# Kernel tuning notes

Measured on AMD Instinct MI355X. Metric: run time of the kernel, lower is better.

Reference implementation:

```python
import jax, jax.numpy as jnp
import numpy as np

N_Q = 5000
MEM = 50
KDIM = 50
VDIM = 200
FC = 50
B = 2048
S = 200


def setup_inputs() -> dict:
    key = jax.random.key(0)
    ks = jax.random.split(key, 14)
    inp = {}
    inp["q_data"] = jax.random.randint(ks[0], (B, S), 0, N_Q, dtype=jnp.int64)
    inp["qa_data"] = jax.random.randint(ks[1], (B, S), 0, 2 * N_Q, dtype=jnp.int64)
    # learned parameters (kaiming-ish random init)
    inp["q_embed_w"] = jax.random.normal(ks[2], (N_Q + 1, KDIM), jnp.float32) * 0.2
    inp["qa_embed_w"] = jax.random.normal(ks[3], (2 * N_Q + 1, VDIM), jnp.float32) * 0.1
    inp["key_memory"] = jax.random.normal(ks[4], (MEM, KDIM), jnp.float32) * 0.2
    inp["init_value_memory"] = jax.random.normal(ks[5], (MEM, VDIM), jnp.float32) * 0.1
    # DKVMN write gates: erase (sigmoid) and add (tanh) transforms of qa embedding
    inp["erase_w"] = jax.random.normal(ks[6], (VDIM, VDIM), jnp.float32) * 0.1
    inp["erase_b"] = jnp.zeros((VDIM,), jnp.float32)
    inp["add_w"] = jax.random.normal(ks[7], (VDIM, VDIM), jnp.float32) * 0.1
    inp["add_b"] = jnp.zeros((VDIM,), jnp.float32)
    # prediction MLP: Linear(VDIM+KDIM -> FC), Tanh, Linear(FC -> 1)
    inp["pred_w1"] = jax.random.normal(ks[8], (VDIM + KDIM, FC), jnp.float32) * 0.1
    inp["pred_b1"] = jnp.zeros((FC,), jnp.float32)
    inp["pred_w2"] = jax.random.normal(ks[9], (FC, 1), jnp.float32) * 0.2
    inp["pred_b2"] = jnp.zeros((1,), jnp.float32)
    return inp


def _dkvmn_forward(q_data, qa_data, q_embed_w, qa_embed_w, key_memory,
                   init_value_memory, erase_w, erase_b, add_w, add_b,
                   pred_w1, pred_b1, pred_w2, pred_b2):
    q_emb = q_embed_w[q_data]    # [B, S, KDIM]
    qa_emb = qa_embed_w[qa_data]  # [B, S, VDIM]
    batch = q_data.shape[0]
    Mv0 = jnp.broadcast_to(init_value_memory, (batch, MEM, VDIM))

    def step(Mv, xs):
        q_t, qa_t = xs  # [B, KDIM], [B, VDIM]
        # attention over memory slots
        w = jax.nn.softmax(q_t @ key_memory.T, axis=-1)          # [B, MEM]
        read = jnp.einsum('bm,bmv->bv', w, Mv)                    # [B, VDIM]
        h = jnp.tanh(jnp.concatenate([read, q_t], -1) @ pred_w1 + pred_b1)
        p = jax.nn.sigmoid((h @ pred_w2 + pred_b2)[:, 0])         # [B]
        # erase/add write
        e = jax.nn.sigmoid(qa_t @ erase_w + erase_b)              # [B, VDIM]
        a = jnp.tanh(qa_t @ add_w + add_b)                        # [B, VDIM]
        Mv_new = Mv * (1.0 - w[:, :, None] * e[:, None, :]) + w[:, :, None] * a[:, None, :]
        return Mv_new, p

    xs = (jnp.swapaxes(q_emb, 0, 1), jnp.swapaxes(qa_emb, 0, 1))  # time-major
    _, preds = jax.lax.scan(step, Mv0, xs)                        # [S, B]
    return preds.T                                                # [B, S]


def reference(q_data, qa_data, q_embed_w, qa_embed_w, key_memory,
              init_value_memory, erase_w, erase_b, add_w, add_b,
              pred_w1, pred_b1, pred_w2, pred_b2):
    preds = _dkvmn_forward(q_data, qa_data, q_embed_w, qa_embed_w, key_memory,
                           init_value_memory, erase_w, erase_b, add_w, add_b,
                           pred_w1, pred_b1, pred_w2, pred_b2)
    zeros = jnp.zeros_like(preds)
    return (preds, zeros, zeros, zeros)
```

## Files before the change

kernel.cpp:

```cpp
#include <hip/hip_runtime.h>
#include <hip/hip_fp16.h>


#define NQ1   5001
#define NQA   10001
#define MEMN  50
#define KD    50
#define VD    200
#define FC    50
#define BB    2048
#define SS    200
#define EA_R  16
#define WHS   28

#define EA_B   626
#define WQ_B   1251
#define PACK_B 8
#define PREP_G (EA_B + WQ_B + PACK_B)

typedef unsigned int   u32;
typedef unsigned short u16;
typedef short    s8v __attribute__((ext_vector_type(8)));
typedef float    f4v __attribute__((ext_vector_type(4)));
typedef _Float16 h2v __attribute__((ext_vector_type(2)));

__device__ __forceinline__ float fast_sigmoid(float x) { return 1.f / (1.f + __expf(-x)); }
__device__ __forceinline__ float fast_tanh(float x) {
    float e2 = __expf(2.f * x);
    return 1.f - 2.f / (e2 + 1.f);
}
__device__ __forceinline__ float bfu16_to_f(u16 u) {
    union { float f; u32 i; } x; x.i = ((u32)u) << 16; return x.f;
}
__device__ __forceinline__ u16 f_to_bfu16(float f) {
    union { float f; u32 i; } x; x.f = f;
    return (u16)((x.i + 0x7fffu + ((x.i >> 16) & 1u)) >> 16);
}
__device__ __forceinline__ h2v u32_to_h2v(u32 u) {
    union { u32 i; h2v h; } x; x.i = u; return x.h;
}
__device__ __forceinline__ u16 f16bits(float f) {
    union { __half h; u16 u; } x; x.h = __float2half(f); return x.u;
}
__device__ __forceinline__ float h16_to_f(u16 u) {
    union { u16 u; __half h; } x; x.u = u; return __half2float(x.h);
}

__global__ __launch_bounds__(256) void prep(
        const float* __restrict__ qemb, const float* __restrict__ km,
        const float* __restrict__ w1,   const float* __restrict__ b1,
        const float* __restrict__ qaemb,
        const float* __restrict__ ew,   const float* __restrict__ ebias,
        const float* __restrict__ aw,   const float* __restrict__ abias,
        float* __restrict__ Wt, u32* __restrict__ Wh, float* __restrict__ Q1,
        u32* __restrict__ EA, u16* __restrict__ W1s,
        float* __restrict__ out_aux) {
    const int tid = threadIdx.x;
    const int blk = blockIdx.x;

    for (size_t i = (size_t)blk * 256 + tid; i < 3ull * BB * SS;
         i += (size_t)PREP_G * 256)
        out_aux[i] = 0.f;

    __shared__ float smem[VD * EA_R];

    if (blk < EA_B) {
        const int r0 = blk * EA_R;
        if (tid < VD) {
            #pragma unroll
            for (int r = 0; r < EA_R; ++r) {
                int row = r0 + r;
                smem[tid * EA_R + r] = (row < NQA) ? qaemb[(size_t)row * VD + tid] : 0.f;
            }
        }
        __syncthreads();
        if (tid >= VD) return;

        float accE[EA_R], accA[EA_R];
        #pragma unroll
        for (int r = 0; r < EA_R; ++r) { accE[r] = 0.f; accA[r] = 0.f; }
        for (int k = 0; k < VD; ++k) {
            float we = ew[k * VD + tid];
            float wa = aw[k * VD + tid];
            #pragma unroll
            for (int r = 0; r < EA_R; ++r) {
                float qv = smem[k * EA_R + r];
                accE[r] = fmaf(qv, we, accE[r]);
                accA[r] = fmaf(qv, wa, accA[r]);
            }
        }
        float be = ebias[tid], ba = abias[tid];
        #pragma unroll
        for (int r = 0; r < EA_R; ++r) {
            int row = r0 + r;
            if (row < NQA) {
                u16 ne16 = f16bits(-fast_sigmoid(accE[r] + be));
                u16 a16  = f16bits(fast_tanh(accA[r] + ba));
                EA[(size_t)row * VD + tid] = (u32)ne16 | ((u32)a16 << 16);
            }
        }
    } else if (blk < EA_B + WQ_B) {
        const int lane = tid & 63;
        const int wv   = tid >> 6;
        const int q    = (blk - EA_B) * 4 + wv;
        const bool qok = q < NQ1;
        float* qrow = smem + wv * 64;
        if (qok && lane < KD) qrow[lane] = qemb[q * KD + lane];
        __syncthreads();
        if (!qok) return;

        float s = -1e30f;
        if (lane < MEMN) {
            s = 0.f;
            #pragma unroll
            for (int k = 0; k < KD; ++k) s = fmaf(qrow[k], km[lane * KD + k], s);
        }
        float mx = s;
        #pragma unroll
        for (int off = 32; off >= 1; off >>= 1) mx = fmaxf(mx, __shfl_xor(mx, off, 64));
        float e = (lane < MEMN) ? __expf(s - mx) : 0.f;
        float sum = e;
        #pragma unroll
        for (int off = 32; off >= 1; off >>= 1) sum += __shfl_xor(sum, off, 64);
        float wv_ = (lane < MEMN) ? (e / sum) : 0.f;
        if (lane < MEMN) Wt[q * MEMN + lane] = wv_;

        float plo = __shfl(wv_, 2 * (lane & 31), 64);
        float phi = __shfl(wv_, 2 * (lane & 31) + 1, 64);
        if (lane < 25) {
            Wh[q * WHS + lane] = (u32)f16bits(plo) | ((u32)f16bits(phi) << 16);
        } else if (lane < WHS) {
            Wh[q * WHS + lane] = 0;
        }

        if (lane < FC) {
            float h = b1[lane];
            #pragma unroll
            for (int k = 0; k < KD; ++k)
                h = fmaf(qrow[k], w1[(VD + k) * FC + lane], h);
            Q1[q * FC + lane] = h;
        }
    } else {
        for (int idx = (blk - EA_B - WQ_B) * 256 + tid; idx < 4 * 7 * 64 * 8;
             idx += PACK_B * 256) {
            int j    = idx & 7;
            int lane = (idx >> 3) & 63;
            int kt   = (idx >> 9) % 7;
            int nt   = idx / 3584;
            int k = kt * 32 + ((lane >> 4) << 3) + j;
            int n = nt * 16 + (lane & 15);
            float v = (k < VD && n < FC) ? w1[k * FC + n] : 0.f;
            W1s[idx] = f_to_bfu16(v);
        }
    }
}

__global__ __launch_bounds__(256) void dkvmn_state(
        const int* __restrict__ qd, const int* __restrict__ qad,
        const u32* __restrict__ Wh, const u32* __restrict__ EA,
        const float* __restrict__ ivm, u16* __restrict__ READ) {
    const int tid = threadIdx.x;
    const int b   = blockIdx.x;
    const int v   = tid;
    const bool active = v < VD;
    const int vc = active ? v : VD - 1;

    h2v mv[25];
    #pragma unroll
    for (int i = 0; i < 25; ++i) {
        mv[i].x = (_Float16)ivm[(2 * i) * VD + vc];
        mv[i].y = (_Float16)ivm[(2 * i + 1) * VD + vc];
    }

    const int base = b * SS;
    int q_c = __builtin_amdgcn_readfirstlane(qd[base]);
    int q_n = __builtin_amdgcn_readfirstlane(qd[base + 1]);
    int qa0 = __builtin_amdgcn_readfirstlane(qad[base]);
    int qa1 = __builtin_amdgcn_readfirstlane(qad[base + 1]);
    u32 ea_c = EA[(size_t)qa0 * VD + vc];
    u32 ea_n = EA[(size_t)qa1 * VD + vc];

    for (int t = 0; t < SS; ++t) {
        int tn = t + 2; tn = (tn < SS) ? tn : (SS - 1);
        int q_nn  = __builtin_amdgcn_readfirstlane(qd[base + tn]);
        int qa_nn = __builtin_amdgcn_readfirstlane(qad[base + tn]);
        u32 ea_nn = EA[(size_t)qa_nn * VD + vc];

        const u32* wrow = Wh + q_c * WHS;
        h2v nev2 = u32_to_h2v(__builtin_amdgcn_perm(ea_c, ea_c, 0x01000100u));
        h2v av2  = u32_to_h2v(__builtin_amdgcn_perm(ea_c, ea_c, 0x03020302u));

        float rdA = 0.f, rdB = 0.f;
        #pragma unroll
        for (int i = 0; i < 25; i += 2) {
            h2v w0 = u32_to_h2v(wrow[i]);
#if __has_builtin(__builtin_amdgcn_fdot2)
            rdA = __builtin_amdgcn_fdot2(w0, mv[i], rdA, false);
#else
            rdA = fmaf((float)w0.x, (float)mv[i].x,
                  fmaf((float)w0.y, (float)mv[i].y, rdA));
#endif
            mv[i] = __builtin_elementwise_fma(
                w0, __builtin_elementwise_fma(nev2, mv[i], av2), mv[i]);
            if (i + 1 < 25) {
                h2v w1p = u32_to_h2v(wrow[i + 1]);
#if __has_builtin(__builtin_amdgcn_fdot2)
                rdB = __builtin_amdgcn_fdot2(w1p, mv[i + 1], rdB, false);
#else
                rdB = fmaf((float)w1p.x, (float)mv[i + 1].x,
                      fmaf((float)w1p.y, (float)mv[i + 1].y, rdB));
#endif
                mv[i + 1] = __builtin_elementwise_fma(
                    w1p, __builtin_elementwise_fma(nev2, mv[i + 1], av2), mv[i + 1]);
            }
        }
        if (active)
            READ[(size_t)(base + t) * VD + v] = f_to_bfu16(rdA + rdB);
        q_c = q_n; q_n = q_nn; ea_c = ea_n; ea_n = ea_nn;
    }
}

__global__ __launch_bounds__(256) void mlp_pred(
        const u16* __restrict__ RD, const int* __restrict__ qd,
        const float* __restrict__ Q1tab, const u16* __restrict__ W1s,
        const float* __restrict__ w2, const float* __restrict__ b2,
        float* __restrict__ out) {
    const int tid  = threadIdx.x;
    const int lane = tid & 63;
    const int wv   = tid >> 6;
    const int strip = blockIdx.x * 4 + wv;
    const int row0  = strip * 16;

    const int mrow = lane & 15;
    const int quad = lane >> 4;

    s8v a[7];
    {
        const u16* arow = RD + (size_t)(row0 + mrow) * VD + quad * 8;
        #pragma unroll
        for (int kt = 0; kt < 7; ++kt)
            a[kt] = *(const s8v*)(arow + kt * 32);
    }

    const float b2f = b2[0];
    float pf[4] = {0.f, 0.f, 0.f, 0.f};

    #pragma unroll
    for (int nt = 0; nt < 4; ++nt) {
        s8v bfr[7];
        #pragma unroll
        for (int kt = 0; kt < 7; ++kt)
            bfr[kt] = *(const s8v*)(W1s + (((nt * 7 + kt) * 64) + lane) * 8);

        f4v acc = {0.f, 0.f, 0.f, 0.f};
        #pragma unroll
        for (int kt = 0; kt < 7; ++kt)
            acc = __builtin_amdgcn_mfma_f32_16x16x32_bf16(a[kt], bfr[kt], acc, 0, 0, 0);

        const int f = nt * 16 + mrow;
        const float w2f = (f < FC) ? w2[f] : 0.f;
        #pragma unroll
        for (int r = 0; r < 4; ++r) {
            int row = row0 + quad * 4 + r;
            float h = acc[r] + Q1tab[qd[row] * FC + f];
            pf[r] = fmaf(fast_tanh(h), w2f, pf[r]);
        }
    }

    #pragma unroll
    for (int r = 0; r < 4; ++r) {
        float s = pf[r];
        s += __shfl_xor(s, 1, 64);
        s += __shfl_xor(s, 2, 64);
        s += __shfl_xor(s, 4, 64);
        s += __shfl_xor(s, 8, 64);
        if (mrow == 0)
            out[row0 + quad * 4 + r] = fast_sigmoid(s + b2f);
    }
}

__global__ void dkvmn_main(const int* __restrict__ qd, const int* __restrict__ qad,
                           const float* __restrict__ Wtab, const float* __restrict__ Q1tab,
                           const u32* __restrict__ EA,
                           const float* __restrict__ ivm,
                           const float* __restrict__ w1,
                           const float* __restrict__ w2,
                           const float* __restrict__ b2,
                           float* __restrict__ out) {
    const int tid  = threadIdx.x;
    const int b    = blockIdx.x;
    const int v    = tid;
    const int lane = tid & 63;
    const int wv   = tid >> 6;

    __shared__ alignas(16) float read_lds[4 * 52];
    __shared__ alignas(16) float part_lds[4 * 52];

    float mv[MEMN];
    if (v < VD) {
        #pragma unroll
        for (int m = 0; m < MEMN; ++m) mv[m] = ivm[m * VD + v];
    }
    float w1r[50];
    if (lane < FC) {
        #pragma unroll
        for (int i = 0; i < 50; ++i) w1r[i] = w1[(wv * 50 + i) * FC + lane];
    } else {
        #pragma unroll
        for (int i = 0; i < 50; ++i) w1r[i] = 0.f;
    }
    const float w2f = (tid < FC) ? w2[tid] : 0.f;
    const float b2f = b2[0];

    const int* qrow_i  = qd  + b * SS;
    const int* qarow_i = qad + b * SS;
    const int jchunk = v / 50;
    const int wslot  = jchunk * 52 + (v - jchunk * 50);

    for (int t = 0; t < SS; ++t) {
        const int q  = __builtin_amdgcn_readfirstlane(qrow_i[t]);
        const int qa = __builtin_amdgcn_readfirstlane(qarow_i[t]);
        const float* wrow = Wtab + q * MEMN;

        u32 ea = 0;
        if (v < VD) ea = EA[(size_t)qa * VD + v];
        float ne = h16_to_f((u16)(ea & 0xffffu));
        float av = h16_to_f((u16)(ea >> 16));

        if (v < VD) {
            float rd0 = 0.f, rd1 = 0.f;
            #pragma unroll
            for (int m = 0; m < MEMN; m += 2) {
                float wm0 = wrow[m], wm1 = wrow[m + 1];
                rd0 = fmaf(wm0, mv[m], rd0);
                mv[m] = fmaf(wm0, fmaf(ne, mv[m], av), mv[m]);
                rd1 = fmaf(wm1, mv[m + 1], rd1);
                mv[m + 1] = fmaf(wm1, fmaf(ne, mv[m + 1], av), mv[m + 1]);
            }
            read_lds[wslot] = rd0 + rd1;
        }
        __syncthreads();

        float part = 0.f;
        {
            const float* rlc = read_lds + wv * 52;
            #pragma unroll
            for (int i = 0; i < 48; i += 4) {
                float4 x = *(const float4*)(rlc + i);
                part = fmaf(x.x, w1r[i],     part);
                part = fmaf(x.y, w1r[i + 1], part);
                part = fmaf(x.z, w1r[i + 2], part);
                part = fmaf(x.w, w1r[i + 3], part);
            }
            part = fmaf(rlc[48], w1r[48], part);
            part = fmaf(rlc[49], w1r[49], part);
        }
        if (lane < FC) part_lds[wv * 52 + lane] = part;
        __syncthreads();

        if (wv == 0) {
            float pf = 0.f;
            if (lane < FC) {
                float h = part_lds[lane] + part_lds[52 + lane] +
                          part_lds[104 + lane] + part_lds[156 + lane] +
                          Q1tab[q * FC + lane];
                pf = fast_tanh(h) * w2f;
            }
            #pragma unroll
            for (int off = 32; off >= 1; off >>= 1) pf += __shfl_xor(pf, off, 64);
            if (lane == 0) out[b * SS + t] = fast_sigmoid(pf + b2f);
        }
    }
}

extern "C" void kernel_launch(void* const* d_in, const int* in_sizes, int n_in,
                              void* d_out, int out_size, void* d_ws, size_t ws_size,
                              hipStream_t stream) {
    const int* qd  = (const int*)d_in[0];
    const int* qad = (const int*)d_in[1];
    const float* qemb  = (const float*)d_in[2];
    const float* qaemb = (const float*)d_in[3];
    const float* km    = (const float*)d_in[4];
    const float* ivm   = (const float*)d_in[5];
    const float* ew    = (const float*)d_in[6];
    const float* eb    = (const float*)d_in[7];
    const float* aw    = (const float*)d_in[8];
    const float* ab    = (const float*)d_in[9];
    const float* w1    = (const float*)d_in[10];
    const float* b1    = (const float*)d_in[11];
    const float* w2    = (const float*)d_in[12];
    const float* b2    = (const float*)d_in[13];
    float* out = (float*)d_out;
    (void)in_sizes; (void)n_in; (void)out_size;

    char* ws = (char*)d_ws;
    float* Wt  = (float*)(ws);
    float* Q1  = (float*)(ws + 1000448);
    u32*   EA  = (u32*)  (ws + 2000896);
    u16*   W1s = (u16*)  (ws + 10001920);
    u32*   Wh  = (u32*)  (ws + 10034688);
    u16*   RD  = (u16*)  (ws + 10595328);
    const size_t need = 10595328ull + 163840000ull + 512ull;

    prep<<<PREP_G, 256, 0, stream>>>(qemb, km, w1, b1, qaemb, ew, eb, aw, ab,
                                     Wt, Wh, Q1, EA, W1s, out + (size_t)BB * SS);

    if (ws_size >= need) {
        dkvmn_state<<<BB, 256, 0, stream>>>(qd, qad, Wh, EA, ivm, RD);
        mlp_pred<<<(BB * SS) / 64, 256, 0, stream>>>(RD, qd, Q1, W1s, w2, b2, out);
    } else {
        dkvmn_main<<<BB, 256, 0, stream>>>(qd, qad, Wt, Q1, EA, ivm, w1, w2, b2, out);
    }
}
```

Measured before the change: 460.8 us.

## Stage index arrays in LDS and prefetch attention rows into registers

The state kernel now loads each block's question and answer indices into shared memory once, instead of issuing scalar global loads every step. The attention weight row for step t+2 is fetched into registers as 16-byte vector loads while steps t and t+1 are computed, using two ping-pong buffers. This is meant to hide global load latency on the serial recurrence, at the cost of more registers per thread (14 uint4) and an LDS read on each step.

```diff
diff --git a/kernel.cpp b/kernel.cpp
--- a/kernel.cpp
+++ b/kernel.cpp
@@ -23,6 +23,7 @@
 typedef short    s8v __attribute__((ext_vector_type(8)));
 typedef float    f4v __attribute__((ext_vector_type(4)));
 typedef _Float16 h2v __attribute__((ext_vector_type(2)));
+typedef u32      u4v __attribute__((ext_vector_type(4)));
 
 __device__ __forceinline__ float fast_sigmoid(float x) { return 1.f / (1.f + __expf(-x)); }
 __device__ __forceinline__ float fast_tanh(float x) {
@@ -165,59 +166,67 @@
     const bool active = v < VD;
     const int vc = active ? v : VD - 1;
 
+    __shared__ int qs_l[SS];
+    __shared__ int qas_l[SS];
+    const int base = b * SS;
+    if (tid < SS) {
+        qs_l[tid]  = qd[base + tid];
+        qas_l[tid] = qad[base + tid];
+    }
+
     h2v mv[25];
     #pragma unroll
     for (int i = 0; i < 25; ++i) {
         mv[i].x = (_Float16)ivm[(2 * i) * VD + vc];
         mv[i].y = (_Float16)ivm[(2 * i + 1) * VD + vc];
     }
-
-    const int base = b * SS;
-    int q_c = __builtin_amdgcn_readfirstlane(qd[base]);
-    int q_n = __builtin_amdgcn_readfirstlane(qd[base + 1]);
-    int qa0 = __builtin_amdgcn_readfirstlane(qad[base]);
-    int qa1 = __builtin_amdgcn_readfirstlane(qad[base + 1]);
-    u32 ea_c = EA[(size_t)qa0 * VD + vc];
-    u32 ea_n = EA[(size_t)qa1 * VD + vc];
-
-    for (int t = 0; t < SS; ++t) {
-        int tn = t + 2; tn = (tn < SS) ? tn : (SS - 1);
-        int q_nn  = __builtin_amdgcn_readfirstlane(qd[base + tn]);
-        int qa_nn = __builtin_amdgcn_readfirstlane(qad[base + tn]);
-        u32 ea_nn = EA[(size_t)qa_nn * VD + vc];
-
-        const u32* wrow = Wh + q_c * WHS;
-        h2v nev2 = u32_to_h2v(__builtin_amdgcn_perm(ea_c, ea_c, 0x01000100u));
-        h2v av2  = u32_to_h2v(__builtin_amdgcn_perm(ea_c, ea_c, 0x03020302u));
-
-        float rdA = 0.f, rdB = 0.f;
-        #pragma unroll
-        for (int i = 0; i < 25; i += 2) {
-            h2v w0 = u32_to_h2v(wrow[i]);
-#if __has_builtin(__builtin_amdgcn_fdot2)
-            rdA = __builtin_amdgcn_fdot2(w0, mv[i], rdA, false);
-#else
-            rdA = fmaf((float)w0.x, (float)mv[i].x,
-                  fmaf((float)w0.y, (float)mv[i].y, rdA));
-#endif
-            mv[i] = __builtin_elementwise_fma(
-                w0, __builtin_elementwise_fma(nev2, mv[i], av2), mv[i]);
-            if (i + 1 < 25) {
-                h2v w1p = u32_to_h2v(wrow[i + 1]);
-#if __has_builtin(__builtin_amdgcn_fdot2)
-                rdB = __builtin_amdgcn_fdot2(w1p, mv[i + 1], rdB, false);
-#else
-                rdB = fmaf((float)w1p.x, (float)mv[i + 1].x,
-                      fmaf((float)w1p.y, (float)mv[i + 1].y, rdB));
-#endif
-                mv[i + 1] = __builtin_elementwise_fma(
-                    w1p, __builtin_elementwise_fma(nev2, mv[i + 1], av2), mv[i + 1]);
-            }
-        }
-        if (active)
-            READ[(size_t)(base + t) * VD + v] = f_to_bfu16(rdA + rdB);
-        q_c = q_n; q_n = q_nn; ea_c = ea_n; ea_n = ea_nn;
-    }
+    __syncthreads();
+
+    u4v wA[7], wB[7];
+    {
+        const u4v* w0 = (const u4v*)(Wh + (size_t)qs_l[0] * WHS);
+        const u4v* w1p = (const u4v*)(Wh + (size_t)qs_l[1] * WHS);
+        #pragma unroll
+        for (int i = 0; i < 7; ++i) wA[i] = w0[i];
+        #pragma unroll
+        for (int i = 0; i < 7; ++i) wB[i] = w1p[i];
+    }
+    u32 ea_c = EA[(size_t)qas_l[0] * VD + vc];
+    u32 ea_n = EA[(size_t)qas_l[1] * VD + vc];
+
+    #define DK_COMPUTE(tc, WCUR, WOTH)                                         \
+    {                                                                          \
+                                         \
+        int tn = (tc) + 2; tn = (tn < SS) ? tn : (SS - 1);                     \
+        u32 ea_nn = EA[(size_t)qas_l[tn] * VD + vc];                           \
+        h2v nev2 = u32_to_h2v(__builtin_amdgcn_perm(ea_c, ea_c, 0x01000100u)); \
+        h2v av2  = u32_to_h2v(__builtin_amdgcn_perm(ea_c, ea_c, 0x03020302u)); \
+        float rdA = 0.f, rdB = 0.f;                                            \
+        _Pragma("unroll")                                                      \
+        for (int i = 0; i < 25; ++i) {                                         \
+            h2v wp = u32_to_h2v(WCUR[i >> 2][i & 3]);                          \
+            if (i & 1) {                                                       \
+                rdB = __builtin_amdgcn_fdot2(wp, mv[i], rdB, false);           \
+            } else {                                                           \
+                rdA = __builtin_amdgcn_fdot2(wp, mv[i], rdA, false);           \
+            }                                                                  \
+            mv[i] = __builtin_elementwise_fma(                                 \
+                wp, __builtin_elementwise_fma(nev2, mv[i], av2), mv[i]);       \
+        }                                                                      \
+        if (active)                                                            \
+            READ[(size_t)(base + (tc)) * VD + v] = f_to_bfu16(rdA + rdB);      \
+        ea_c = ea_n; ea_n = ea_nn;                                             \
+                    \
+        const u4v* wrn = (const u4v*)(Wh + (size_t)qs_l[tn] * WHS);            \
+        _Pragma("unroll")                                                      \
+        for (int i = 0; i < 7; ++i) WOTH[i] = wrn[i];                          \
+    }
+
+    for (int t = 0; t < SS; t += 2) {
+        DK_COMPUTE(t,     wA, wA);
+        DK_COMPUTE(t + 1, wB, wB);
+    }
+    #undef DK_COMPUTE
 }
 
 __global__ __launch_bounds__(256) void mlp_pred(
```

Measured after the change: 468.6 us. Within noise of the previous version (+1.7%).
